# Optimization experiments

Hardware: AMD Instinct MI355X
Metric: run time of the kernel (lower is better)

Reference implementation:

```python
import jax, jax.numpy as jnp
import numpy as np

TEMP_MIN, TEMP_MAX = 0.1, 1.0
NEG = -1e30  # finite stand-in for -inf (grad-safe)


def _cumlse(x, axis, reverse=False):
    # cumulative logsumexp along `axis`
    return jax.lax.associative_scan(jnp.logaddexp, x, axis=axis, reverse=reverse)


def setup_inputs() -> dict:
    key = jax.random.key(0)
    k1, k2, k3 = jax.random.split(key, 3)
    B, T, M, C = 16, 512, 2048, 512
    return {
        "text_embeddings": jax.random.normal(k1, (B, T, C), jnp.float32),
        "mel_embeddings": jax.random.normal(k2, (B, M, C), jnp.float32),
        "noise_uniform": jax.random.uniform(k3, (B, T, M), jnp.float32, 1e-6, 1.0 - 1e-6),
        "temperature_ratio": jnp.full((1,), 0.5, jnp.float32),
    }


def reference(text_embeddings, mel_embeddings, noise_uniform, temperature_ratio):
    B, T, C = text_embeddings.shape
    M, Cm = mel_embeddings.shape[1], mel_embeddings.shape[2]
    energy = jnp.einsum('btc,bmc->btm', text_embeddings, mel_embeddings) / np.float32(np.sqrt(C * Cm))
    temperature = TEMP_MIN + (TEMP_MAX - TEMP_MIN) * jnp.reshape(temperature_ratio, ())
    gumbel = -jnp.log(-jnp.log(noise_uniform))
    # torch code computes e = exp((energy+noise)/T); we keep it in log domain:
    log_e = (energy + gumbel) / temperature                      # [B,T,M]
    # log_cond_prob[b,t,k,j] = log_e[b,t,k] - log_S[b,t,j] if k>=j else -inf
    # (the torch 4D triu-masked tensor, never materialized here)
    log_S = _cumlse(log_e, axis=2, reverse=True)                 # log sum_{k>=j} e[b,t,k]

    # alpha DP: alpha[b,i,k+1] = lse_{j<=k}(alpha[b,i-1,j] + lcp[b,i-1,k,j])
    #         = log_e[b,i-1,k] + lse_{j<=k}(alpha[b,i-1,j] - log_S[b,i-1,j])
    alpha0 = jnp.concatenate([jnp.zeros((B, 1), log_e.dtype),
                              jnp.full((B, M), NEG, log_e.dtype)], axis=1)  # [B,M+1]
    def alpha_step(prev, xs):
        le_t, ls_t = xs                                          # [B,M] each
        inner = _cumlse(prev[:, :M] - ls_t, axis=1)              # lse over j<=k
        new = jnp.concatenate([jnp.full((B, 1), NEG, le_t.dtype), le_t + inner], axis=1)
        return new, new
    _, alphas = jax.lax.scan(alpha_step, alpha0,
                             (jnp.swapaxes(log_e, 0, 1), jnp.swapaxes(log_S, 0, 1)))
    alpha_tail = jnp.swapaxes(alphas, 0, 1)[:, :, 1:]            # alpha[:,1:,1:] -> [B,T,M]

    # beta DP (intended backward recurrence; torch source had an undefined
    # `cond_prob` and a shape bug here):
    # beta[b,i,j] = lse_{k>=j}(beta[b,i+1,k] + log_e[b,i,k]) - log_S[b,i,j]
    beta_T = jnp.zeros((B, M), log_e.dtype).at[:, M - 1].set(1.0)  # faithful odd init =1
    def beta_step(nxt, xs):
        le_t, ls_t = xs
        new = _cumlse(nxt + le_t, axis=1, reverse=True) - ls_t
        return new, new
    _, betas = jax.lax.scan(beta_step, beta_T,
                            (jnp.swapaxes(log_e, 0, 1)[:T - 1], jnp.swapaxes(log_S, 0, 1)[:T - 1]),
                            reverse=True)
    beta = jnp.swapaxes(jnp.concatenate([betas, beta_T[None]], axis=0), 0, 1)  # [B,T,M]

    gamma = alpha_tail + beta
    gamma_log = gamma - jax.scipy.special.logsumexp(gamma, axis=1, keepdims=True)
    # torch uses raw (log-domain) gamma in the bmm; kept faithful
    expanded = jnp.einsum('btm,btc->bmc', gamma, text_embeddings)  # [B,M,C]
    return gamma_log, expanded
```

## Files before the change

### kernel.cpp

```cpp
#include <hip/hip_runtime.h>

#define B_  16
#define T_  512
#define M_  2048
#define C_  512
#define NEGV (-1e30f)
#define L2E 1.4426950408889634f
#define LN2 0.69314718055994531f

typedef unsigned short u16;
typedef unsigned int   u32;
using bf16x8 = __attribute__((ext_vector_type(8))) short;
using f32x4  = __attribute__((ext_vector_type(4))) float;

__device__ __forceinline__ u16 f2bf(float x) {
  u32 u = __float_as_uint(x);
  return (u16)((u + 0x7FFFu + ((u >> 16) & 1u)) >> 16);
}
__device__ __forceinline__ float bf2f(u16 u) {
  return __uint_as_float(((u32)u) << 16);
}
__device__ __forceinline__ float rdlane63(float x) {
  return __int_as_float(__builtin_amdgcn_readlane(__float_as_int(x), 63));
}

__device__ __forceinline__ float wscan_add(float x) {
  x += __int_as_float(__builtin_amdgcn_update_dpp(0, __float_as_int(x), 0x111, 0xF, 0xF, true));
  x += __int_as_float(__builtin_amdgcn_update_dpp(0, __float_as_int(x), 0x112, 0xF, 0xF, true));
  x += __int_as_float(__builtin_amdgcn_update_dpp(0, __float_as_int(x), 0x114, 0xF, 0xF, true));
  x += __int_as_float(__builtin_amdgcn_update_dpp(0, __float_as_int(x), 0x118, 0xF, 0xF, true));
  x += __int_as_float(__builtin_amdgcn_update_dpp(0, __float_as_int(x), 0x142, 0xA, 0xF, true));
  x += __int_as_float(__builtin_amdgcn_update_dpp(0, __float_as_int(x), 0x143, 0xC, 0xF, true));
  return x;
}
__device__ __forceinline__ float dpp_shr1(float x) {
  return __int_as_float(__builtin_amdgcn_update_dpp(0, __float_as_int(x), 0x138, 0xF, 0xF, true));
}

__launch_bounds__(256)
__global__ void k1_energy(const float* __restrict__ text, const float* __restrict__ mel,
                          const float* __restrict__ noise, const float* __restrict__ ratio,
                          u16* __restrict__ ttbuf)
{
  __shared__ __align__(16) short As[128][40];
  __shared__ __align__(16) short Bs[128][40];
  const int b   = blockIdx.z;
  const int t0  = blockIdx.x * 128;
  const int m0  = blockIdx.y * 128;
  const int tid = threadIdx.x;
  const int lane = tid & 63, wid = tid >> 6;
  const int wr = wid >> 1, wc = wid & 1;
  const float* Ab = text + (size_t)b * T_ * C_;
  const float* Bb = mel  + (size_t)b * M_ * C_;
  f32x4 acc[4][4];
#pragma unroll
  for (int i = 0; i < 4; ++i)
#pragma unroll
    for (int j = 0; j < 4; ++j) acc[i][j] = (f32x4){0.f, 0.f, 0.f, 0.f};

  const int kq = (tid & 7) * 4;
  const int rb = tid >> 3;
  for (int kk = 0; kk < C_; kk += 32) {
    __syncthreads();
#pragma unroll
    for (int it = 0; it < 4; ++it) {
      int r = rb + it * 32;
      float4 va = *(const float4*)(Ab + (size_t)(t0 + r) * C_ + kk + kq);
      As[r][kq + 0] = (short)f2bf(va.x); As[r][kq + 1] = (short)f2bf(va.y);
      As[r][kq + 2] = (short)f2bf(va.z); As[r][kq + 3] = (short)f2bf(va.w);
      float4 vb = *(const float4*)(Bb + (size_t)(m0 + r) * C_ + kk + kq);
      Bs[r][kq + 0] = (short)f2bf(vb.x); Bs[r][kq + 1] = (short)f2bf(vb.y);
      Bs[r][kq + 2] = (short)f2bf(vb.z); Bs[r][kq + 3] = (short)f2bf(vb.w);
    }
    __syncthreads();
    const int k0 = (lane >> 4) * 8;
    bf16x8 af[4], bfr[4];
#pragma unroll
    for (int i = 0; i < 4; ++i) {
      af[i]  = *(const bf16x8*)&As[wr * 64 + i * 16 + (lane & 15)][k0];
      bfr[i] = *(const bf16x8*)&Bs[wc * 64 + i * 16 + (lane & 15)][k0];
    }
#pragma unroll
    for (int i = 0; i < 4; ++i)
#pragma unroll
      for (int j = 0; j < 4; ++j)
        acc[i][j] = __builtin_amdgcn_mfma_f32_16x16x32_bf16(af[i], bfr[j], acc[i][j], 0, 0, 0);
  }
  const float invT = 1.0f / (0.1f + 0.9f * ratio[0]);
  const float D2 = 14.5f * invT * L2E;
#pragma unroll
  for (int i = 0; i < 4; ++i) {
#pragma unroll
    for (int j = 0; j < 4; ++j) {
#pragma unroll
      for (int rr = 0; rr < 4; ++rr) {
        int t = t0 + wr * 64 + i * 16 + (lane >> 4) * 4 + rr;
        int m = m0 + wc * 64 + j * 16 + (lane & 15);
        size_t idx = ((size_t)b * T_ + t) * M_ + m;
        float en = acc[i][j][rr] * (1.0f / 512.0f);
        float u  = noise[idx];
        float nl = -LN2 * __builtin_amdgcn_logf(u);
        float g  = -LN2 * __builtin_amdgcn_logf(nl);
        float le = (en + g) * invT;
        float tv = __builtin_amdgcn_exp2f(__builtin_fmaf(le, L2E, -D2));
        ttbuf[idx] = f2bf(tv);
      }
    }
  }
}

__launch_bounds__(256)
__global__ void k2u(const u16* __restrict__ tt, u16* __restrict__ W,
                    u16* __restrict__ UA, u16* __restrict__ UB,
                    u16* __restrict__ Qb, float* __restrict__ r00)
{
  __shared__ float part0[4], part1[4];
  const size_t row = blockIdx.x;
  const int t = (int)(row & (T_ - 1));
  const int b = (int)(row >> 9);
  const size_t rowN = (t < T_ - 1) ? row + 1 : row;
  const int tid = threadIdx.x, lane = tid & 63, wid = tid >> 6;
  const int c0 = tid * 8;
  const u16* ttr = tt + row * M_ + c0;
  const u16* ttn = tt + rowN * M_ + c0;
  float x[8], y[8];
  { uint4 wa = *(const uint4*)ttr;
    x[0]=__uint_as_float(wa.x<<16); x[1]=__uint_as_float(wa.x&0xFFFF0000u);
    x[2]=__uint_as_float(wa.y<<16); x[3]=__uint_as_float(wa.y&0xFFFF0000u);
    x[4]=__uint_as_float(wa.z<<16); x[5]=__uint_as_float(wa.z&0xFFFF0000u);
    x[6]=__uint_as_float(wa.w<<16); x[7]=__uint_as_float(wa.w&0xFFFF0000u); }
  { uint4 wb = *(const uint4*)ttn;
    y[0]=__uint_as_float(wb.x<<16); y[1]=__uint_as_float(wb.x&0xFFFF0000u);
    y[2]=__uint_as_float(wb.y<<16); y[3]=__uint_as_float(wb.y&0xFFFF0000u);
    y[4]=__uint_as_float(wb.z<<16); y[5]=__uint_as_float(wb.z&0xFFFF0000u);
    y[6]=__uint_as_float(wb.w<<16); y[7]=__uint_as_float(wb.w&0xFFFF0000u); }
  float xm1 = (c0 == 0) ? 0.f : bf2f(ttr[-1]);

  float sx[8], sy[8];
  sx[7] = x[7]; sy[7] = y[7];
#pragma unroll
  for (int i = 6; i >= 0; --i) { sx[i] = x[i] + sx[i+1]; sy[i] = y[i] + sy[i+1]; }
  float vx = sx[0], vy = sy[0];
#pragma unroll
  for (int d = 1; d < 64; d <<= 1) {
    float tx = __shfl_down(vx, d), ty = __shfl_down(vy, d);
    if (lane < 64 - d) { vx += tx; vy += ty; }
  }
  float ex = __shfl_down(vx, 1), ey = __shfl_down(vy, 1);
  if (lane == 63) { ex = 0.f; ey = 0.f; }
  if (lane == 0) { part0[wid] = vx; part1[wid] = vy; }
  __syncthreads();
  float wex = 0.f, wey = 0.f;
  for (int w2 = wid + 1; w2 < 4; ++w2) { wex += part0[w2]; wey += part1[w2]; }
  float offx = ex + wex, offy = ey + wey;

  float rx[8], ry[8];
#pragma unroll
  for (int i = 0; i < 8; ++i) {
    rx[i] = __builtin_amdgcn_rcpf(sx[i] + offx);
    ry[i] = __builtin_amdgcn_rcpf(sy[i] + offy);
  }
  { u32 o[4];
#pragma unroll
    for (int i = 0; i < 4; ++i)
      o[i] = __builtin_amdgcn_perm(__float_as_uint(x[2*i+1]*rx[2*i+1]),
                                   __float_as_uint(x[2*i]*rx[2*i]), 0x07060302u);
    *(uint4*)(W + row * M_ + c0) = make_uint4(o[0],o[1],o[2],o[3]); }

  if (t == 0 && tid == 0) r00[b] = rx[0];

  if (t == T_ - 1) {
    float q[8];
#pragma unroll
    for (int i = 0; i < 8; ++i) q[i] = sx[i] + offx;
    if (tid == 255) q[7] *= 2.718281828f;
    u32 o[4];
#pragma unroll
    for (int i = 0; i < 4; ++i)
      o[i] = __builtin_amdgcn_perm(__float_as_uint(q[2*i+1]), __float_as_uint(q[2*i]), 0x07060302u);
    *(uint4*)(Qb + ((size_t)b * T_ + T_ - 1) * M_ + c0) = make_uint4(o[0],o[1],o[2],o[3]);
  } else {
    u32 o[4];
#pragma unroll
    for (int i = 0; i < 4; ++i)
      o[i] = __builtin_amdgcn_perm(__float_as_uint(x[2*i+1]*ry[2*i+1]),
                                   __float_as_uint(x[2*i]*ry[2*i]), 0x07060302u);
    *(uint4*)(UB + row * M_ + c0) = make_uint4(o[0],o[1],o[2],o[3]);
    float ua[8];
    ua[0] = xm1 * ry[0];
#pragma unroll
    for (int i = 1; i < 8; ++i) ua[i] = x[i-1] * ry[i];
#pragma unroll
    for (int i = 0; i < 4; ++i)
      o[i] = __builtin_amdgcn_perm(__float_as_uint(ua[2*i+1]), __float_as_uint(ua[2*i]), 0x07060302u);
    *(uint4*)(UA + (row + 1) * M_ + c0) = make_uint4(o[0],o[1],o[2],o[3]);
  }
}

__launch_bounds__(512)
__global__ void k3a_partial(const float* __restrict__ text, float* __restrict__ partial)
{
  const int b = blockIdx.x >> 3, ch = blockIdx.x & 7, c = threadIdx.x;
  const float* tb = text + (size_t)b * T_ * C_ + (size_t)ch * 64 * C_ + c;
  float s = 0.f;
#pragma unroll 8
  for (int tt = 0; tt < 64; ++tt) s += tb[(size_t)tt * C_];
  partial[((size_t)b * 8 + ch) * C_ + c] = s;
}

__launch_bounds__(512)
__global__ void k3b_suffix(const float* __restrict__ text, const float* __restrict__ partial,
                           float* __restrict__ suffix)
{
  const int b = blockIdx.x >> 3, ch = blockIdx.x & 7, c = threadIdx.x;
  float off = 0.f;
  for (int ch2 = ch + 1; ch2 < 8; ++ch2) off += partial[((size_t)b * 8 + ch2) * C_ + c];
  const float* tb = text + (size_t)b * T_ * C_ + (size_t)ch * 64 * C_ + c;
  float* sb = suffix + (size_t)b * (T_ + 1) * C_ + (size_t)ch * 64 * C_ + c;
  if (ch == 7) sb[(size_t)64 * C_] = 0.f;
  float s = off;
  for (int tt = 63; tt >= 0; --tt) {
    s += tb[(size_t)tt * C_];
    sb[(size_t)tt * C_] = s;
  }
}

__launch_bounds__(256)
__global__ void k3t_textT(const float* __restrict__ text, u16* __restrict__ textT)
{
  __shared__ u16 tile[64][66];
  const int b  = blockIdx.z;
  const int t0 = blockIdx.x * 64;
  const int c0 = blockIdx.y * 64;
  const int tid = threadIdx.x;
  const int j = tid & 63, i4 = tid >> 6;
#pragma unroll
  for (int it = 0; it < 16; ++it) {
    int i = it * 4 + i4;
    tile[i][j] = f2bf(text[((size_t)b * T_ + t0 + i) * C_ + c0 + j]);
  }
  __syncthreads();
#pragma unroll
  for (int it = 0; it < 16; ++it) {
    int cc = it * 4 + i4;
    textT[((size_t)b * C_ + c0 + cc) * T_ + t0 + j] = tile[j][cc];
  }
}

__launch_bounds__(64, 1)
__global__ void k4_dp(const u16* __restrict__ UA, const u16* __restrict__ UB,
                      const float* __restrict__ r00,
                      u16* __restrict__ Abuf, u16* __restrict__ Bbuf,
                      float* __restrict__ CAa, float* __restrict__ CBa)
{
  const int blk = blockIdx.x;
  const int b   = blk & 15;
  const int lane = threadIdx.x & 63;
  uint4 raw[2][4];
  float cum[32], Pv[32];
  float Cv;

  if (blk < 16) {
    const int c0 = lane * 32;
    const u16* Up = UA + (size_t)b * T_ * M_;
    u16* AO = Abuf + (size_t)b * T_ * M_;
    float* CO = CAa + (size_t)b * T_;

#define TLDA(BUF, R) { const uint4* p_ = (const uint4*)(Up + (size_t)(R) * M_ + c0); \
    raw[BUF][0]=p_[0]; raw[BUF][1]=p_[1]; raw[BUF][2]=p_[2]; raw[BUF][3]=p_[3]; }

#define AF2(E, W_) { \
    cum[E]     = __uint_as_float((W_) << 16)         * Pv[(E)-1]; \
    cum[(E)+1] = __uint_as_float((W_) & 0xFFFF0000u) * Pv[E]; }

#define ASTEP(BUF, RIDX) { \
    const int r_ = (RIDX); \
    { float pm1 = dpp_shr1(Pv[31]); \
      u32 w0 = raw[BUF][0].x; \
      cum[0] = __uint_as_float(w0 << 16) * pm1; \
      cum[1] = __uint_as_float(w0 & 0xFFFF0000u) * Pv[0]; } \
    AF2(2,  raw[BUF][0].y) AF2(4,  raw[BUF][0].z) AF2(6,  raw[BUF][0].w) \
    AF2(8,  raw[BUF][1].x) AF2(10, raw[BUF][1].y) AF2(12, raw[BUF][1].z) AF2(14, raw[BUF][1].w) \
    AF2(16, raw[BUF][2].x) AF2(18, raw[BUF][2].y) AF2(20, raw[BUF][2].z) AF2(22, raw[BUF][2].w) \
    AF2(24, raw[BUF][3].x) AF2(26, raw[BUF][3].y) AF2(28, raw[BUF][3].z) AF2(30, raw[BUF][3].w) \
    _Pragma("unroll") for (int c = 0; c < 4; ++c) \
      _Pragma("unroll") for (int k = 1; k < 8; ++k) cum[8*c+k] += cum[8*c+k-1]; \
    { float lt = (cum[7] + cum[15]) + (cum[23] + cum[31]); \
      float v_ = wscan_add(lt); \
      float exw = v_ - lt; \
      float Zt = rdlane63(v_); \
      float f0 = exw, f1 = f0 + cum[7], f2 = f1 + cum[15], f3 = f2 + cum[23]; \
      float Zc = fmaxf(Zt, 1e-35f); \
      float zr = __builtin_amdgcn_rcpf(Zc); \
      Cv += LN2 * __builtin_amdgcn_logf(Zc); \
      if (lane == 0) CO[r_] = Cv; \
      float fz0 = f0*zr, fz1 = f1*zr, fz2 = f2*zr, fz3 = f3*zr; \
      _Pragma("unroll") for (int k = 0; k < 8; ++k) { \
        Pv[k]    = __builtin_fmaf(cum[k],    zr, fz0); \
        Pv[8+k]  = __builtin_fmaf(cum[8+k],  zr, fz1); \
        Pv[16+k] = __builtin_fmaf(cum[16+k], zr, fz2); \
        Pv[24+k] = __builtin_fmaf(cum[24+k], zr, fz3); } } \
    { u32 w_[16]; \
      _Pragma("unroll") for (int d = 0; d < 16; ++d) \
        w_[d] = __builtin_amdgcn_perm(__float_as_uint(Pv[2*d+1]), __float_as_uint(Pv[2*d]), 0x07060302u); \
      uint4* op = (uint4*)(AO + (size_t)r_ * M_ + c0); \
      op[0] = make_uint4(w_[0],w_[1],w_[2],w_[3]); \
      op[1] = make_uint4(w_[4],w_[5],w_[6],w_[7]); \
      op[2] = make_uint4(w_[8],w_[9],w_[10],w_[11]); \
      op[3] = make_uint4(w_[12],w_[13],w_[14],w_[15]); } \
    TLDA(BUF, (r_ + 2 < T_) ? r_ + 2 : T_ - 1) \
    __builtin_amdgcn_sched_barrier(0); \
  }

    { uint4 one4 = make_uint4(0x3F803F80u, 0x3F803F80u, 0x3F803F80u, 0x3F803F80u);
      uint4* op = (uint4*)(AO + c0);
      op[0] = one4; op[1] = one4; op[2] = one4; op[3] = one4; }
    Cv = LN2 * __builtin_amdgcn_logf(r00[b]);
    if (lane == 0) CO[0] = Cv;
#pragma unroll
    for (int e = 0; e < 32; ++e) Pv[e] = 1.0f;

    TLDA(0, 1) TLDA(1, 2)
    for (int r = 1; r + 1 < T_; r += 2) {
      ASTEP(0, r)
      ASTEP(1, r + 1)
    }
    ASTEP(0, T_ - 1)
  } else {
    const int jb = M_ - 32 - lane * 32;
    const u16* Up = UB + (size_t)b * T_ * M_;
    u16* BO = Bbuf + (size_t)b * T_ * M_;
    float* CO = CBa + (size_t)b * T_;

#define TLDB(BUF, R) { const uint4* p_ = (const uint4*)(Up + (size_t)(R) * M_ + jb); \
    raw[BUF][0]=p_[0]; raw[BUF][1]=p_[1]; raw[BUF][2]=p_[2]; raw[BUF][3]=p_[3]; }

#define BF2(E, W_) { \
    cum[E]     = __uint_as_float((W_) << 16)         * Pv[E]; \
    cum[(E)+1] = __uint_as_float((W_) & 0xFFFF0000u) * Pv[(E)+1]; }

#define BSTEP(BUF, TIDX) { \
    const int t_ = (TIDX); \
    BF2(0,  raw[BUF][0].x) BF2(2,  raw[BUF][0].y) BF2(4,  raw[BUF][0].z) BF2(6,  raw[BUF][0].w) \
    BF2(8,  raw[BUF][1].x) BF2(10, raw[BUF][1].y) BF2(12, raw[BUF][1].z) BF2(14, raw[BUF][1].w) \
    BF2(16, raw[BUF][2].x) BF2(18, raw[BUF][2].y) BF2(20, raw[BUF][2].z) BF2(22, raw[BUF][2].w) \
    BF2(24, raw[BUF][3].x) BF2(26, raw[BUF][3].y) BF2(28, raw[BUF][3].z) BF2(30, raw[BUF][3].w) \
    _Pragma("unroll") for (int c = 0; c < 4; ++c) \
      _Pragma("unroll") for (int k = 6; k >= 0; --k) cum[8*c+k] += cum[8*c+k+1]; \
    { float lt = (cum[0] + cum[8]) + (cum[16] + cum[24]); \
      float v_ = wscan_add(lt); \
      float exw = v_ - lt; \
      float Zb = rdlane63(v_); \
      float f0 = exw, f1 = f0 + cum[24], f2 = f1 + cum[16], f3 = f2 + cum[8]; \
      float Zc = fmaxf(Zb, 1e-35f); \
      float zr = __builtin_amdgcn_rcpf(Zc); \
      Cv += LN2 * __builtin_amdgcn_logf(Zc); \
      if (lane == 0) CO[t_] = Cv; \
      float fz0 = f0*zr, fz1 = f1*zr, fz2 = f2*zr, fz3 = f3*zr; \
      _Pragma("unroll") for (int k = 0; k < 8; ++k) { \
        Pv[24+k] = __builtin_fmaf(cum[24+k], zr, fz0); \
        Pv[16+k] = __builtin_fmaf(cum[16+k], zr, fz1); \
        Pv[8+k]  = __builtin_fmaf(cum[8+k],  zr, fz2); \
        Pv[k]    = __builtin_fmaf(cum[k],    zr, fz3); } } \
    { u32 w_[16]; \
      _Pragma("unroll") for (int d = 0; d < 16; ++d) \
        w_[d] = __builtin_amdgcn_perm(__float_as_uint(Pv[2*d+1]), __float_as_uint(Pv[2*d]), 0x07060302u); \
      uint4* op = (uint4*)(BO + (size_t)t_ * M_ + jb); \
      op[0] = make_uint4(w_[0],w_[1],w_[2],w_[3]); \
      op[1] = make_uint4(w_[4],w_[5],w_[6],w_[7]); \
      op[2] = make_uint4(w_[8],w_[9],w_[10],w_[11]); \
      op[3] = make_uint4(w_[12],w_[13],w_[14],w_[15]); } \
    TLDB(BUF, (t_ - 2 >= 0) ? t_ - 2 : 0) \
    __builtin_amdgcn_sched_barrier(0); \
  }

    { const uint4* ip = (const uint4*)(BO + (size_t)(T_ - 1) * M_ + jb);
      uint4 q0 = ip[0], q1 = ip[1], q2 = ip[2], q3 = ip[3];
      Pv[0]=__uint_as_float(q0.x<<16);  Pv[1]=__uint_as_float(q0.x&0xFFFF0000u);
      Pv[2]=__uint_as_float(q0.y<<16);  Pv[3]=__uint_as_float(q0.y&0xFFFF0000u);
      Pv[4]=__uint_as_float(q0.z<<16);  Pv[5]=__uint_as_float(q0.z&0xFFFF0000u);
      Pv[6]=__uint_as_float(q0.w<<16);  Pv[7]=__uint_as_float(q0.w&0xFFFF0000u);
      Pv[8]=__uint_as_float(q1.x<<16);  Pv[9]=__uint_as_float(q1.x&0xFFFF0000u);
      Pv[10]=__uint_as_float(q1.y<<16); Pv[11]=__uint_as_float(q1.y&0xFFFF0000u);
      Pv[12]=__uint_as_float(q1.z<<16); Pv[13]=__uint_as_float(q1.z&0xFFFF0000u);
      Pv[14]=__uint_as_float(q1.w<<16); Pv[15]=__uint_as_float(q1.w&0xFFFF0000u);
      Pv[16]=__uint_as_float(q2.x<<16); Pv[17]=__uint_as_float(q2.x&0xFFFF0000u);
      Pv[18]=__uint_as_float(q2.y<<16); Pv[19]=__uint_as_float(q2.y&0xFFFF0000u);
      Pv[20]=__uint_as_float(q2.z<<16); Pv[21]=__uint_as_float(q2.z&0xFFFF0000u);
      Pv[22]=__uint_as_float(q2.w<<16); Pv[23]=__uint_as_float(q2.w&0xFFFF0000u);
      Pv[24]=__uint_as_float(q3.x<<16); Pv[25]=__uint_as_float(q3.x&0xFFFF0000u);
      Pv[26]=__uint_as_float(q3.y<<16); Pv[27]=__uint_as_float(q3.y&0xFFFF0000u);
      Pv[28]=__uint_as_float(q3.z<<16); Pv[29]=__uint_as_float(q3.z&0xFFFF0000u);
      Pv[30]=__uint_as_float(q3.w<<16); Pv[31]=__uint_as_float(q3.w&0xFFFF0000u); }
    Cv = 0.f;
    if (lane == 0) CO[T_ - 1] = 0.f;

    TLDB(0, T_ - 2) TLDB(1, T_ - 3)
    for (int t = T_ - 2; t >= 2; t -= 2) {
      BSTEP(0, t)
      BSTEP(1, t - 1)
    }
    BSTEP(0, 0)
  }
}

__launch_bounds__(256)
__global__ void k6_combine(const u16* __restrict__ Pb, const u16* __restrict__ Qb,
                           const u16* __restrict__ Wb,
                           const float* __restrict__ CAa, const float* __restrict__ CBa,
                           float* __restrict__ gamma_log, u16* __restrict__ gammaT)
{
  __shared__ u16 gst[32][514];
  __shared__ float cd[T_];
  __shared__ float smx[8][32], ssm[8][32];
  const int b  = blockIdx.x >> 6;
  const int m0 = (blockIdx.x & 63) * 32;
  const int tid = threadIdx.x;
  const int mi = tid & 31, ti = tid >> 5;
  const int m = m0 + mi;
  const size_t base = (size_t)b * T_ * M_ + m;

  cd[tid]       = CAa[b * T_ + tid]       + CBa[b * T_ + tid];
  cd[tid + 256] = CAa[b * T_ + tid + 256] + CBa[b * T_ + tid + 256];
  __syncthreads();

  float mx = -3.0e38f, s = 0.f;
  for (int t = ti; t < T_; t += 8) {
    float p  = bf2f(Pb[base + (size_t)t * M_]);
    float q  = bf2f(Qb[base + (size_t)t * M_]);
    float wv = bf2f(Wb[base + (size_t)t * M_]);
    float g;
    if (t <= m) {
      g = __builtin_fmaf(__builtin_amdgcn_logf(p * q * wv), LN2, cd[t]);
      g = fmaxf(g, -1e8f);
    } else g = NEGV;
    gst[mi][t] = f2bf(g);
    if (g > mx) { s = s * __builtin_amdgcn_exp2f((mx - g) * L2E) + 1.f; mx = g; }
    else        { s += __builtin_amdgcn_exp2f((g - mx) * L2E); }
  }
  smx[ti][mi] = mx; ssm[ti][mi] = s;
  __syncthreads();
  float Mv = smx[0][mi], Sv = ssm[0][mi];
#pragma unroll
  for (int k = 1; k < 8; ++k) {
    float Mk = smx[k][mi], Sk = ssm[k][mi];
    if (Mk > Mv) { Sv = Sv * __builtin_amdgcn_exp2f((Mv - Mk) * L2E) + Sk; Mv = Mk; }
    else         { Sv += Sk * __builtin_amdgcn_exp2f((Mk - Mv) * L2E); }
  }
  const float lse = Mv + LN2 * __builtin_amdgcn_logf(Sv);

  for (int t = ti; t < T_; t += 8) {
    float g = (t <= m) ? bf2f(gst[mi][t]) : NEGV;
    gamma_log[base + (size_t)t * M_] = g - lse;
  }
  for (int k = 0; k < 32; ++k) {
    u32 val = *(const u32*)&gst[k][2 * tid];
    int mr = m0 + k;
    u32 lo = (2 * tid     <= mr) ? (val & 0x0000FFFFu) : 0u;
    u32 hi = (2 * tid + 1 <= mr) ? (val & 0xFFFF0000u) : 0u;
    ((u32*)gammaT)[((((size_t)b * M_ + m0 + k) * T_) >> 1) + tid] = lo | hi;
  }
}

__launch_bounds__(256)
__global__ void k7_expanded(const u16* __restrict__ gammaT, const u16* __restrict__ textT,
                            const float* __restrict__ suffix, float* __restrict__ expanded)
{
  __shared__ __align__(16) short As[128][40];
  __shared__ __align__(16) short Bs[128][40];
  const int b   = blockIdx.z;
  const int m0  = blockIdx.x * 128;
  const int c0  = blockIdx.y * 128;
  const int tid = threadIdx.x;
  const int lane = tid & 63, wid = tid >> 6;
  const int wr = wid >> 1, wc = wid & 1;
  const u16* Ab = gammaT + (size_t)b * M_ * T_;
  const u16* Bb = textT  + (size_t)b * C_ * T_;
  f32x4 acc[4][4];
#pragma unroll
  for (int i = 0; i < 4; ++i)
#pragma unroll
    for (int j = 0; j < 4; ++j) acc[i][j] = (f32x4){0.f, 0.f, 0.f, 0.f};

  const int ko  = (tid & 3) * 8;
  const int rb2 = tid >> 2;
  for (int kk = 0; kk < T_; kk += 32) {
    __syncthreads();
#pragma unroll
    for (int it = 0; it < 2; ++it) {
      int r = rb2 + it * 64;
      *(uint4*)&As[r][ko] = *(const uint4*)(Ab + (size_t)(m0 + r) * T_ + kk + ko);
      *(uint4*)&Bs[r][ko] = *(const uint4*)(Bb + (size_t)(c0 + r) * T_ + kk + ko);
    }
    __syncthreads();
    const int k0 = (lane >> 4) * 8;
    bf16x8 af[4], bfr[4];
#pragma unroll
    for (int i = 0; i < 4; ++i) {
      af[i]  = *(const bf16x8*)&As[wr * 64 + i * 16 + (lane & 15)][k0];
      bfr[i] = *(const bf16x8*)&Bs[wc * 64 + i * 16 + (lane & 15)][k0];
    }
#pragma unroll
    for (int i = 0; i < 4; ++i)
#pragma unroll
      for (int j = 0; j < 4; ++j)
        acc[i][j] = __builtin_amdgcn_mfma_f32_16x16x32_bf16(af[i], bfr[j], acc[i][j], 0, 0, 0);
  }
#pragma unroll
  for (int i = 0; i < 4; ++i) {
#pragma unroll
    for (int j = 0; j < 4; ++j) {
#pragma unroll
      for (int rr = 0; rr < 4; ++rr) {
        int m = m0 + wr * 64 + i * 16 + (lane >> 4) * 4 + rr;
        int c = c0 + wc * 64 + j * 16 + (lane & 15);
        int sidx = (m + 1 < T_) ? (m + 1) : T_;
        float sfx = suffix[((size_t)b * (T_ + 1) + sidx) * C_ + c];
        expanded[((size_t)b * M_ + m) * C_ + c] = acc[i][j][rr] + NEGV * sfx;
      }
    }
  }
}

extern "C" void kernel_launch(void* const* d_in, const int* in_sizes, int n_in,
                              void* d_out, int out_size, void* d_ws, size_t ws_size,
                              hipStream_t stream) {
  const float* text  = (const float*)d_in[0];
  const float* mel   = (const float*)d_in[1];
  const float* noise = (const float*)d_in[2];
  const float* ratio = (const float*)d_in[3];

  const size_t BTM = (size_t)B_ * T_ * M_;
  float* out       = (float*)d_out;
  float* gamma_log = out;
  float* expanded  = out + BTM;

  char* w = (char*)d_ws;
  u16*   ttbuf  = (u16*)  (w + 0);
  u16*   Abuf   = (u16*)  (w + 33554432);
  u16*   Wb     = (u16*)  (w + 67108864);
  u16*   UA     = (u16*)  (w + 100663296);
  u16*   UB     = (u16*)  (w + 134217728);
  float* suffix = (float*)(w + 167772160);
  u16*   textT  = (u16*)  (w + 184582144);
  u16*   gammaT = (u16*)  (w + 0);
  float* partial = (float*)(w + 67108864);
  u16*   Bbuf = (u16*)expanded;
  float* CAa  = (float*)((char*)expanded + 33554432);
  float* CBa  = CAa + (size_t)B_ * T_;
  float* r00  = CBa + (size_t)B_ * T_;

  k3a_partial<<<B_ * 8,          512, 0, stream>>>(text, partial);
  k3b_suffix <<<B_ * 8,          512, 0, stream>>>(text, partial, suffix);
  k3t_textT  <<<dim3(8, 8, 16),  256, 0, stream>>>(text, textT);
  k1_energy  <<<dim3(4, 16, 16), 256, 0, stream>>>(text, mel, noise, ratio, ttbuf);
  k2u        <<<B_ * T_,         256, 0, stream>>>(ttbuf, Wb, UA, UB, Bbuf, r00);
  k4_dp      <<<32,               64, 0, stream>>>(UA, UB, r00, Abuf, Bbuf, CAa, CBa);
  k6_combine <<<B_ * 64,         256, 0, stream>>>(Abuf, Bbuf, Wb, CAa, CBa, gamma_log, gammaT);
  k7_expanded<<<dim3(16, 4, 16), 256, 0, stream>>>(gammaT, textT, suffix, expanded);
}
```

Before: 457.9 us.

## Add producer wave prefetching DP input rows into double-buffered LDS

The serial DP kernel now runs two waves per block. A producer wave streams groups of six input rows into a double-buffered LDS area with global_load_lds. The compute wave reads each row from LDS instead of using its own two-deep register prefetch from global memory. The goal is to hide global load latency behind the serial 512-step recurrence with a deeper prefetch. In exchange it adds a block barrier every six steps, extra LDS reads, and depends on the async LDS loads being complete at each barrier.

```diff
diff --git a/kernel.cpp b/kernel.cpp
--- a/kernel.cpp
+++ b/kernel.cpp
@@ -7,6 +7,8 @@
 #define NEGV (-1e30f)
 #define L2E 1.4426950408889634f
 #define LN2 0.69314718055994531f
+#define GRP 6
+#define NG  86
 
 typedef unsigned short u16;
 typedef unsigned int   u32;
@@ -247,42 +249,70 @@
   }
 }
 
-__launch_bounds__(64, 1)
+__launch_bounds__(128, 1)
 __global__ void k4_dp(const u16* __restrict__ UA, const u16* __restrict__ UB,
                       const float* __restrict__ r00,
                       u16* __restrict__ Abuf, u16* __restrict__ Bbuf,
                       float* __restrict__ CAa, float* __restrict__ CBa)
 {
+  __shared__ __align__(16) char ldsraw[2 * GRP * 4096];
   const int blk = blockIdx.x;
   const int b   = blk & 15;
-  const int lane = threadIdx.x & 63;
-  uint4 raw[2][4];
+  const int tid = threadIdx.x;
+  const int lane = tid & 63;
+  const int wv   = tid >> 6;
   float cum[32], Pv[32];
   float Cv;
 
+#define PISSUE(RP_, BB, SLOT) { \
+    const u16* rp_ = (RP_) + lane * 32; \
+    char* lb_ = ldsraw + (((BB) * GRP + (SLOT)) * 4096); \
+    __builtin_amdgcn_global_load_lds((const __attribute__((address_space(1))) void*)(rp_ + 0),  (__attribute__((address_space(3))) void*)(lb_ + 0),    16, 0, 0); \
+    __builtin_amdgcn_global_load_lds((const __attribute__((address_space(1))) void*)(rp_ + 8),  (__attribute__((address_space(3))) void*)(lb_ + 1024), 16, 0, 0); \
+    __builtin_amdgcn_global_load_lds((const __attribute__((address_space(1))) void*)(rp_ + 16), (__attribute__((address_space(3))) void*)(lb_ + 2048), 16, 0, 0); \
+    __builtin_amdgcn_global_load_lds((const __attribute__((address_space(1))) void*)(rp_ + 24), (__attribute__((address_space(3))) void*)(lb_ + 3072), 16, 0, 0); }
+
   if (blk < 16) {
-    const int c0 = lane * 32;
     const u16* Up = UA + (size_t)b * T_ * M_;
+
+    if (wv == 1) {
+      for (int s = 0; s < GRP; ++s) {
+        int r = 1 + s; if (r > T_ - 1) r = T_ - 1;
+        PISSUE(Up + (size_t)r * M_, 0, s)
+      }
+      for (int g = 0; g < NG; ++g) {
+        __syncthreads();
+        if (g + 1 < NG) {
+          for (int s = 0; s < GRP; ++s) {
+            int r = 1 + (g + 1) * GRP + s; if (r > T_ - 1) r = T_ - 1;
+            PISSUE(Up + (size_t)r * M_, (g + 1) & 1, s)
+          }
+        }
+      }
+      return;
+    }
+
     u16* AO = Abuf + (size_t)b * T_ * M_;
     float* CO = CAa + (size_t)b * T_;
-
-#define TLDA(BUF, R) { const uint4* p_ = (const uint4*)(Up + (size_t)(R) * M_ + c0); \
-    raw[BUF][0]=p_[0]; raw[BUF][1]=p_[1]; raw[BUF][2]=p_[2]; raw[BUF][3]=p_[3]; }
 
 #define AF2(E, W_) { \
     cum[E]     = __uint_as_float((W_) << 16)         * Pv[(E)-1]; \
     cum[(E)+1] = __uint_as_float((W_) & 0xFFFF0000u) * Pv[E]; }
 
-#define ASTEP(BUF, RIDX) { \
+#define ASTEP_L(LB_, RIDX) { \
     const int r_ = (RIDX); \
+    const char* lb_ = (LB_); \
+    uint4 rw0 = *(const uint4*)(lb_ + lane * 16); \
+    uint4 rw1 = *(const uint4*)(lb_ + 1024 + lane * 16); \
+    uint4 rw2 = *(const uint4*)(lb_ + 2048 + lane * 16); \
+    uint4 rw3 = *(const uint4*)(lb_ + 3072 + lane * 16); \
     { float pm1 = dpp_shr1(Pv[31]); \
-      u32 w0 = raw[BUF][0].x; \
-      cum[0] = __uint_as_float(w0 << 16) * pm1; \
-      cum[1] = __uint_as_float(w0 & 0xFFFF0000u) * Pv[0]; } \
-    AF2(2,  raw[BUF][0].y) AF2(4,  raw[BUF][0].z) AF2(6,  raw[BUF][0].w) \
-    AF2(8,  raw[BUF][1].x) AF2(10, raw[BUF][1].y) AF2(12, raw[BUF][1].z) AF2(14, raw[BUF][1].w) \
-    AF2(16, raw[BUF][2].x) AF2(18, raw[BUF][2].y) AF2(20, raw[BUF][2].z) AF2(22, raw[BUF][2].w) \
-    AF2(24, raw[BUF][3].x) AF2(26, raw[BUF][3].y) AF2(28, raw[BUF][3].z) AF2(30, raw[BUF][3].w) \
+      cum[0] = __uint_as_float(rw0.x << 16) * pm1; \
+      cum[1] = __uint_as_float(rw0.x & 0xFFFF0000u) * Pv[0]; } \
+    AF2(2,  rw0.y) AF2(4,  rw0.z) AF2(6,  rw0.w) \
+    AF2(8,  rw1.x) AF2(10, rw1.y) AF2(12, rw1.z) AF2(14, rw1.w) \
+    AF2(16, rw2.x) AF2(18, rw2.y) AF2(20, rw2.z) AF2(22, rw2.w) \
+    AF2(24, rw3.x) AF2(26, rw3.y) AF2(28, rw3.z) AF2(30, rw3.w) \
     _Pragma("unroll") for (int c = 0; c < 4; ++c) \
       _Pragma("unroll") for (int k = 1; k < 8; ++k) cum[8*c+k] += cum[8*c+k-1]; \
     { float lt = (cum[7] + cum[15]) + (cum[23] + cum[31]); \
@@ -303,48 +333,69 @@
     { u32 w_[16]; \
       _Pragma("unroll") for (int d = 0; d < 16; ++d) \
         w_[d] = __builtin_amdgcn_perm(__float_as_uint(Pv[2*d+1]), __float_as_uint(Pv[2*d]), 0x07060302u); \
-      uint4* op = (uint4*)(AO + (size_t)r_ * M_ + c0); \
+      uint4* op = (uint4*)(AO + (size_t)r_ * M_ + lane * 32); \
       op[0] = make_uint4(w_[0],w_[1],w_[2],w_[3]); \
       op[1] = make_uint4(w_[4],w_[5],w_[6],w_[7]); \
       op[2] = make_uint4(w_[8],w_[9],w_[10],w_[11]); \
       op[3] = make_uint4(w_[12],w_[13],w_[14],w_[15]); } \
-    TLDA(BUF, (r_ + 2 < T_) ? r_ + 2 : T_ - 1) \
-    __builtin_amdgcn_sched_barrier(0); \
   }
 
     { uint4 one4 = make_uint4(0x3F803F80u, 0x3F803F80u, 0x3F803F80u, 0x3F803F80u);
-      uint4* op = (uint4*)(AO + c0);
+      uint4* op = (uint4*)(AO + lane * 32);
       op[0] = one4; op[1] = one4; op[2] = one4; op[3] = one4; }
     Cv = LN2 * __builtin_amdgcn_logf(r00[b]);
     if (lane == 0) CO[0] = Cv;
 #pragma unroll
     for (int e = 0; e < 32; ++e) Pv[e] = 1.0f;
 
-    TLDA(0, 1) TLDA(1, 2)
-    for (int r = 1; r + 1 < T_; r += 2) {
-      ASTEP(0, r)
-      ASTEP(1, r + 1)
-    }
-    ASTEP(0, T_ - 1)
+    for (int g = 0; g < NG; ++g) {
+      __syncthreads();
+      const char* gb = ldsraw + ((g & 1) * GRP) * 4096;
+#pragma unroll
+      for (int s = 0; s < GRP; ++s) {
+        int r = 1 + g * GRP + s;
+        if (r < T_) { ASTEP_L(gb + s * 4096, r) }
+      }
+    }
   } else {
+    const u16* Up = UB + (size_t)b * T_ * M_;
+
+    if (wv == 1) {
+      for (int s = 0; s < GRP; ++s) {
+        int t = 510 - s; if (t < 0) t = 0;
+        PISSUE(Up + (size_t)t * M_, 0, s)
+      }
+      for (int g = 0; g < NG; ++g) {
+        __syncthreads();
+        if (g + 1 < NG) {
+          for (int s = 0; s < GRP; ++s) {
+            int t = 510 - ((g + 1) * GRP + s); if (t < 0) t = 0;
+            PISSUE(Up + (size_t)t * M_, (g + 1) & 1, s)
+          }
+        }
+      }
+      return;
+    }
+
     const int jb = M_ - 32 - lane * 32;
-    const u16* Up = UB + (size_t)b * T_ * M_;
     u16* BO = Bbuf + (size_t)b * T_ * M_;
     float* CO = CBa + (size_t)b * T_;
-
-#define TLDB(BUF, R) { const uint4* p_ = (const uint4*)(Up + (size_t)(R) * M_ + jb); \
-    raw[BUF][0]=p_[0]; raw[BUF][1]=p_[1]; raw[BUF][2]=p_[2]; raw[BUF][3]=p_[3]; }
 
 #define BF2(E, W_) { \
     cum[E]     = __uint_as_float((W_) << 16)         * Pv[E]; \
     cum[(E)+1] = __uint_as_float((W_) & 0xFFFF0000u) * Pv[(E)+1]; }
 
-#define BSTEP(BUF, TIDX) { \
+#define BSTEP_L(LB_, TIDX) { \
     const int t_ = (TIDX); \
-    BF2(0,  raw[BUF][0].x) BF2(2,  raw[BUF][0].y) BF2(4,  raw[BUF][0].z) BF2(6,  raw[BUF][0].w) \
-    BF2(8,  raw[BUF][1].x) BF2(10, raw[BUF][1].y) BF2(12, raw[BUF][1].z) BF2(14, raw[BUF][1].w) \
-    BF2(16, raw[BUF][2].x) BF2(18, raw[BUF][2].y) BF2(20, raw[BUF][2].z) BF2(22, raw[BUF][2].w) \
-    BF2(24, raw[BUF][3].x) BF2(26, raw[BUF][3].y) BF2(28, raw[BUF][3].z) BF2(30, raw[BUF][3].w) \
+    const char* lb_ = (LB_); \
+    uint4 rw0 = *(const uint4*)(lb_ + (63 - lane) * 16); \
+    uint4 rw1 = *(const uint4*)(lb_ + 1024 + (63 - lane) * 16); \
+    uint4 rw2 = *(const uint4*)(lb_ + 2048 + (63 - lane) * 16); \
+    uint4 rw3 = *(const uint4*)(lb_ + 3072 + (63 - lane) * 16); \
+    BF2(0,  rw0.x) BF2(2,  rw0.y) BF2(4,  rw0.z) BF2(6,  rw0.w) \
+    BF2(8,  rw1.x) BF2(10, rw1.y) BF2(12, rw1.z) BF2(14, rw1.w) \
+    BF2(16, rw2.x) BF2(18, rw2.y) BF2(20, rw2.z) BF2(22, rw2.w) \
+    BF2(24, rw3.x) BF2(26, rw3.y) BF2(28, rw3.z) BF2(30, rw3.w) \
     _Pragma("unroll") for (int c = 0; c < 4; ++c) \
       _Pragma("unroll") for (int k = 6; k >= 0; --k) cum[8*c+k] += cum[8*c+k+1]; \
     { float lt = (cum[0] + cum[8]) + (cum[16] + cum[24]); \
@@ -370,8 +421,6 @@
       op[1] = make_uint4(w_[4],w_[5],w_[6],w_[7]); \
       op[2] = make_uint4(w_[8],w_[9],w_[10],w_[11]); \
       op[3] = make_uint4(w_[12],w_[13],w_[14],w_[15]); } \
-    TLDB(BUF, (t_ - 2 >= 0) ? t_ - 2 : 0) \
-    __builtin_amdgcn_sched_barrier(0); \
   }
 
     { const uint4* ip = (const uint4*)(BO + (size_t)(T_ - 1) * M_ + jb);
@@ -395,12 +444,15 @@
     Cv = 0.f;
     if (lane == 0) CO[T_ - 1] = 0.f;
 
-    TLDB(0, T_ - 2) TLDB(1, T_ - 3)
-    for (int t = T_ - 2; t >= 2; t -= 2) {
-      BSTEP(0, t)
-      BSTEP(1, t - 1)
-    }
-    BSTEP(0, 0)
+    for (int g = 0; g < NG; ++g) {
+      __syncthreads();
+      const char* gb = ldsraw + ((g & 1) * GRP) * 4096;
+#pragma unroll
+      for (int s = 0; s < GRP; ++s) {
+        int t = 510 - (g * GRP + s);
+        if (t >= 0) { BSTEP_L(gb + s * 4096, t) }
+      }
+    }
   }
 }
 
@@ -555,7 +607,7 @@
   k3t_textT  <<<dim3(8, 8, 16),  256, 0, stream>>>(text, textT);
   k1_energy  <<<dim3(4, 16, 16), 256, 0, stream>>>(text, mel, noise, ratio, ttbuf);
   k2u        <<<B_ * T_,         256, 0, stream>>>(ttbuf, Wb, UA, UB, Bbuf, r00);
-  k4_dp      <<<32,               64, 0, stream>>>(UA, UB, r00, Abuf, Bbuf, CAa, CBa);
+  k4_dp      <<<32,              128, 0, stream>>>(UA, UB, r00, Abuf, Bbuf, CAa, CBa);
   k6_combine <<<B_ * 64,         256, 0, stream>>>(Abuf, Bbuf, Wb, CAa, CBa, gamma_log, gammaT);
   k7_expanded<<<dim3(16, 4, 16), 256, 0, stream>>>(gammaT, textT, suffix, expanded);
 }
```

Result: faster. 412.2 us (-10.0%).
